# Kernel optimization log

Measured on AMD Instinct MI355X. Metric: run time of the kernel, lower is better.

The kernel has to match this reference:

```python
import jax, jax.numpy as jnp
import numpy as np

B, C, H, W, K = 4, 32, 192, 192, 3
BETA = 15.0   # soft-max temperature used by the repo's Morphology module
EPS = 1e-5    # BatchNorm eps
KK = K * K


def _window_taps(x, dil):
    """Zero-padded dilated KxK window taps, stacked on axis 0 -> (KK, B, C, H, W).
    Matches nn.Unfold(kernel_size=K, dilation=dil, padding=dil*(K//2))."""
    p = dil * (K // 2)
    xp = jnp.pad(x, ((0, 0), (0, 0), (p, p), (p, p)))
    return jnp.stack(
        [xp[:, :, i * dil:i * dil + H, j * dil:j * dil + W]
         for i in range(K) for j in range(K)], axis=0)


def _w_taps(w):
    # (C, K, K) -> (KK, 1, C, 1, 1) aligned with tap order i*K+j
    return w.reshape(C, KK).T[:, None, :, None, None]


def soft_dilate(x, w, dil):
    v = _window_taps(x, dil) + _w_taps(w)          # (KK,B,C,H,W)
    return jax.nn.logsumexp(BETA * v, axis=0) / BETA


def soft_erode(x, w, dil):
    v = _w_taps(w) - _window_taps(x, dil)
    return -(jax.nn.logsumexp(BETA * v, axis=0) / BETA)


def batchnorm(x, gamma, beta):
    mu = jnp.mean(x, axis=(0, 2, 3), keepdims=True)
    var = jnp.var(x, axis=(0, 2, 3), keepdims=True)
    xn = (x - mu) * jax.lax.rsqrt(var + EPS)
    return xn * gamma[None, :, None, None] + beta[None, :, None, None]


def setup_inputs() -> dict:
    key = jax.random.key(0)
    k1, k2, k3, k4 = jax.random.split(key, 4)
    return {
        "x": jax.random.normal(k1, (B, C, H, W), jnp.float32),
        "wd": jax.random.normal(k2, (4, C, K, K), jnp.float32) * 0.1,
        "we": jax.random.normal(k3, (4, C, K, K), jnp.float32) * 0.1,
        "gs": jnp.ones((4, C), jnp.float32),
        "bs": jnp.zeros((4, C), jnp.float32),
        "Wc": jax.random.normal(k4, (C, 4 * C), jnp.float32) * (1.0 / np.sqrt(4 * C)),
        "g": jnp.ones((C,), jnp.float32),
        "b": jnp.zeros((C,), jnp.float32),
    }


def reference(x, wd, we, gs, bs, Wc, g, b):
    branches = []
    for i in range(4):                      # fixed set of dilation factors 1..4
        d = i + 1
        y = soft_dilate(x, wd[i], d)        # soft morphological dilation
        y = soft_erode(y, we[i], d)         # then erosion => closing
        y = jax.nn.relu(batchnorm(y, gs[i], bs[i]))
        branches.append(y)
    xc = jnp.concatenate(branches, axis=1)  # (B, 4C, H, W)
    y = jnp.einsum('bihw,oi->bohw', xc, Wc) # 1x1 conv, no bias
    y = jax.nn.relu(batchnorm(y, g, b))
    return y                                 # Dropout2d is identity in eval
```

## Files before the change

kernel.cpp:

```cpp
#include <hip/hip_runtime.h>
#include <hip/hip_bf16.h>

#define B_   4
#define C_   32
#define H_   192
#define W_   192
#define HW_  (H_ * W_)
#define EPS_ 1e-5f

#define SCALE_IN  21.640425613334453f
#define SCALE_OUT 0.046209812037329687f

#define SPW 48
#define SQW 40

#define NP1 (128 * 288)
#define NP2 (32 * 288)

__device__ __forceinline__ float bf2f(unsigned short u) {
    return __uint_as_float((unsigned int)u << 16);
}
__device__ __forceinline__ unsigned short f2bf(float f) {
    const unsigned int u = __float_as_uint(f);
    return (unsigned short)((u + 0x7fffu + ((u >> 16) & 1u)) >> 16);
}

__device__ float          g_cw[2304];
__device__ float          g_Wt[4096];
__device__ float          g_stats[320];
__device__ float          g_p1[2 * NP1];
__device__ float          g_p2[2 * NP2];
__device__ __attribute__((aligned(16))) unsigned short g_E[(size_t)4 * B_ * C_ * HW_];
__device__ __attribute__((aligned(16))) unsigned short g_Yb[(size_t)B_ * C_ * HW_];

__global__ void prep_k(const float* __restrict__ wd, const float* __restrict__ we,
                       const float* __restrict__ Wc) {
    for (int i = threadIdx.x; i < 2304; i += 256) {
        const float v = (i < 1152) ? wd[i] : we[i - 1152];
        g_cw[i] = exp2f(SCALE_IN * v);
    }
    for (int i = threadIdx.x; i < 4096; i += 256) {
        const int ci = i >> 5;
        const int k  = i & 31;
        g_Wt[i] = Wc[(size_t)k * 128 + ci];
    }
}

template<int D>
__device__ __forceinline__ void morph_branch(int b, int c, int h0, int w0,
                                             int slotbase,
                                             const float* __restrict__ sP,
                                             float* __restrict__ sQ) {
    constexpr int QE    = 32 + 2 * D;
    constexpr int QEG8  = (QE + 7) / 8;
    constexpr int UNITS = QE * QEG8;
    constexpr int POFF  = 8 - 2 * D;
    constexpr int AB    = POFF & ~3;
    constexpr int OFF   = POFF & 3;
    constexpr int NR    = (OFF + 2 * D + 8 + 3) / 4;
    constexpr int NR3   = (2 * D + 8 + 3) / 4;
    constexpr int br    = D - 1;

    const int tid = threadIdx.x;
    const int cb  = (br * C_ + c) * 9;

    if (tid < UNITS) {
        float cd[9];
#pragma unroll
        for (int k = 0; k < 9; k++) cd[k] = g_cw[cb + k];

        const int qi = tid / QEG8;
        const int qj = (tid - qi * QEG8) * 8;
        float a[8];
#pragma unroll
        for (int u = 0; u < 8; u++) a[u] = 0.f;

#pragma unroll
        for (int i = 0; i < 3; i++) {
            const float* rp = &sP[(qi + 8 + (i - 2) * D) * SPW + qj + AB];
            float buf[NR * 4];
#pragma unroll
            for (int r = 0; r < NR; r++)
                *(float4*)&buf[r * 4] = *(const float4*)&rp[r * 4];
#pragma unroll
            for (int j = 0; j < 3; j++) {
                const float wgt = cd[i * 3 + j];
#pragma unroll
                for (int u = 0; u < 8; u++)
                    a[u] = fmaf(wgt, buf[OFF + j * D + u], a[u]);
            }
        }
        const int hq = h0 - D + qi;
        const bool rowo = (hq < 0) || (hq >= H_);
        float q[8];
#pragma unroll
        for (int u = 0; u < 8; u++) {
            float qq = __builtin_amdgcn_rcpf(a[u]);
            const int wq = w0 - D + qj + u;
            q[u] = (rowo || (wq < 0) || (wq >= W_)) ? 1.0f : qq;
        }
        *(float4*)&sQ[qi * SQW + qj]     = make_float4(q[0], q[1], q[2], q[3]);
        *(float4*)&sQ[qi * SQW + qj + 4] = make_float4(q[4], q[5], q[6], q[7]);
    }
    __syncthreads();

    if (tid < 128) {
        float ce[9];
#pragma unroll
        for (int k = 0; k < 9; k++) ce[k] = g_cw[1152 + cb + k];

        const int oi = tid >> 2;
        const int oj = (tid & 3) * 8;
        float t[8];
#pragma unroll
        for (int u = 0; u < 8; u++) t[u] = 0.f;

#pragma unroll
        for (int i = 0; i < 3; i++) {
            const float* rq = &sQ[(oi + i * D) * SQW + oj];
            float buf[NR3 * 4];
#pragma unroll
            for (int r = 0; r < NR3; r++)
                *(float4*)&buf[r * 4] = *(const float4*)&rq[r * 4];
#pragma unroll
            for (int j = 0; j < 3; j++) {
                const float wgt = ce[i * 3 + j];
#pragma unroll
                for (int u = 0; u < 8; u++)
                    t[u] = fmaf(wgt, buf[j * D + u], t[u]);
            }
        }
        float e[8];
#pragma unroll
        for (int u = 0; u < 8; u++) e[u] = -SCALE_OUT * log2f(t[u]);

        uint4 pk;
        pk.x = (unsigned int)f2bf(e[0]) | ((unsigned int)f2bf(e[1]) << 16);
        pk.y = (unsigned int)f2bf(e[2]) | ((unsigned int)f2bf(e[3]) << 16);
        pk.z = (unsigned int)f2bf(e[4]) | ((unsigned int)f2bf(e[5]) << 16);
        pk.w = (unsigned int)f2bf(e[6]) | ((unsigned int)f2bf(e[7]) << 16);
        *(uint4*)&g_E[(((size_t)br * B_ + b) * C_ + c) * HW_
                      + (size_t)(h0 + oi) * W_ + w0 + oj] = pk;

        float s1 = 0.f, s2 = 0.f;
#pragma unroll
        for (int u = 0; u < 8; u++) { s1 += e[u]; s2 += e[u] * e[u]; }
#pragma unroll
        for (int off = 32; off >= 1; off >>= 1) {
            s1 += __shfl_down(s1, off, 64);
            s2 += __shfl_down(s2, off, 64);
        }
        if ((tid & 63) == 0) {
            const int slot = (br * C_ + c) * 288 + slotbase + (tid >> 6);
            g_p1[slot]       = s1;
            g_p1[NP1 + slot] = s2;
        }
    }
    __syncthreads();
}

__global__ __launch_bounds__(256) void morph_k(const float* __restrict__ x) {
    __shared__ float sP[48 * SPW];
    __shared__ float sQ[40 * SQW];
    const int tile = blockIdx.x;
    const int c    = blockIdx.y;
    const int b    = blockIdx.z;
    const int th   = tile / 6;
    const int tw   = tile - th * 6;
    const int h0   = th * 32, w0 = tw * 32;

    const float* xm = x + (size_t)(b * C_ + c) * HW_;
    for (int idx = threadIdx.x; idx < 48 * 48; idx += 256) {
        const int r  = idx / 48, q = idx - r * 48;
        const int ih = h0 - 8 + r, iw = w0 - 8 + q;
        const int ihc = min(max(ih, 0), H_ - 1);
        const int iwc = min(max(iw, 0), W_ - 1);
        const float xv = xm[ihc * W_ + iwc];
        const bool inb = (ih == ihc) && (iw == iwc);
        sP[r * SPW + q] = inb ? exp2f(SCALE_IN * xv) : 1.0f;
    }
    __syncthreads();

    const int slotbase = (b * 36 + tile) * 2;
    morph_branch<1>(b, c, h0, w0, slotbase, sP, sQ);
    morph_branch<2>(b, c, h0, w0, slotbase, sP, sQ);
    morph_branch<3>(b, c, h0, w0, slotbase, sP, sQ);
    morph_branch<4>(b, c, h0, w0, slotbase, sP, sQ);
}

__global__ __launch_bounds__(256) void fin1_k(const float* __restrict__ gs,
                                              const float* __restrict__ bs) {
    const int chan = blockIdx.x;
    const int base = chan * 288;
    float s1 = 0.0f, s2 = 0.0f;
    for (int i = threadIdx.x; i < 288; i += 256) {
        s1 += g_p1[base + i];
        s2 += g_p1[NP1 + base + i];
    }
#pragma unroll
    for (int off = 32; off >= 1; off >>= 1) {
        s1 += __shfl_down(s1, off, 64);
        s2 += __shfl_down(s2, off, 64);
    }
    __shared__ float l1[4], l2[4];
    const int lane = threadIdx.x & 63;
    const int wv   = threadIdx.x >> 6;
    if (lane == 0) { l1[wv] = s1; l2[wv] = s2; }
    __syncthreads();
    if (threadIdx.x == 0) {
        const float S1 = l1[0] + l1[1] + l1[2] + l1[3];
        const float S2 = l2[0] + l2[1] + l2[2] + l2[3];
        const float N  = (float)(B_ * HW_);
        const float mu = S1 / N;
        const float va = fmaxf(S2 / N - mu * mu, 0.0f);
        const float sc = gs[chan] * rsqrtf(va + EPS_);
        g_stats[chan]       = sc;
        g_stats[128 + chan] = bs[chan] - mu * sc;
    }
}

__global__ __launch_bounds__(256) void conv_k(void) {
    const int og = blockIdx.y;
    const int b  = blockIdx.z;
    const int p  = (blockIdx.x * 256 + threadIdx.x) * 2;

    float acc0[8], acc1[8];
#pragma unroll
    for (int k = 0; k < 8; k++) { acc0[k] = 0.0f; acc1[k] = 0.0f; }

#pragma unroll 8
    for (int ci = 0; ci < 128; ci++) {
        const int br = ci >> 5;
        const int c  = ci & 31;
        const unsigned int eu =
            *(const unsigned int*)&g_E[(((size_t)br * B_ + b) * C_ + c) * HW_ + p];
        float v0 = __uint_as_float(eu << 16);
        float v1 = __uint_as_float(eu & 0xffff0000u);
        const float sc = g_stats[ci], sh = g_stats[128 + ci];
        v0 = fmaxf(fmaf(v0, sc, sh), 0.0f);
        v1 = fmaxf(fmaf(v1, sc, sh), 0.0f);
        const float* wr = &g_Wt[ci * 32 + og * 8];
#pragma unroll
        for (int k = 0; k < 8; k++) {
            acc0[k] = fmaf(v0, wr[k], acc0[k]);
            acc1[k] = fmaf(v1, wr[k], acc1[k]);
        }
    }

    unsigned short* Yp = g_Yb + ((size_t)b * C_ + og * 8) * HW_ + p;
#pragma unroll
    for (int k = 0; k < 8; k++) {
        const unsigned int pack =
            (unsigned int)f2bf(acc0[k]) | ((unsigned int)f2bf(acc1[k]) << 16);
        *(unsigned int*)&Yp[(size_t)k * HW_] = pack;
    }

    __shared__ float l1[8][4], l2[8][4];
    const int lane = threadIdx.x & 63;
    const int wv   = threadIdx.x >> 6;
#pragma unroll
    for (int k = 0; k < 8; k++) {
        float s1 = acc0[k] + acc1[k];
        float s2 = acc0[k] * acc0[k] + acc1[k] * acc1[k];
#pragma unroll
        for (int off = 32; off >= 1; off >>= 1) {
            s1 += __shfl_down(s1, off, 64);
            s2 += __shfl_down(s2, off, 64);
        }
        if (lane == 0) { l1[k][wv] = s1; l2[k][wv] = s2; }
    }
    __syncthreads();
    if (threadIdx.x < 8) {
        const int k = threadIdx.x;
        const int chan = og * 8 + k;
        const int slot = chan * 288 + b * 72 + blockIdx.x;
        g_p2[slot]       = l1[k][0] + l1[k][1] + l1[k][2] + l1[k][3];
        g_p2[NP2 + slot] = l2[k][0] + l2[k][1] + l2[k][2] + l2[k][3];
    }
}

__global__ __launch_bounds__(256) void fin2_k(const float* __restrict__ g,
                                              const float* __restrict__ bb) {
    const int chan = blockIdx.x;
    const int base = chan * 288;
    float s1 = 0.0f, s2 = 0.0f;
    for (int i = threadIdx.x; i < 288; i += 256) {
        s1 += g_p2[base + i];
        s2 += g_p2[NP2 + base + i];
    }
#pragma unroll
    for (int off = 32; off >= 1; off >>= 1) {
        s1 += __shfl_down(s1, off, 64);
        s2 += __shfl_down(s2, off, 64);
    }
    __shared__ float l1[4], l2[4];
    const int lane = threadIdx.x & 63;
    const int wv   = threadIdx.x >> 6;
    if (lane == 0) { l1[wv] = s1; l2[wv] = s2; }
    __syncthreads();
    if (threadIdx.x == 0) {
        const float S1 = l1[0] + l1[1] + l1[2] + l1[3];
        const float S2 = l2[0] + l2[1] + l2[2] + l2[3];
        const float N  = (float)(B_ * HW_);
        const float mu = S1 / N;
        const float va = fmaxf(S2 / N - mu * mu, 0.0f);
        const float sc = g[chan] * rsqrtf(va + EPS_);
        g_stats[256 + chan] = sc;
        g_stats[288 + chan] = bb[chan] - mu * sc;
    }
}

__global__ __launch_bounds__(256) void final_k(float* __restrict__ out) {
    const int c = blockIdx.y;
    const int b = blockIdx.z;
    const size_t base = (size_t)(b * C_ + c) * HW_ + (blockIdx.x * 256 + threadIdx.x) * 8;
    const float sc = g_stats[256 + c];
    const float sh = g_stats[288 + c];
    const uint4 u = *(const uint4*)&g_Yb[base];

    float4 r0, r1;
    r0.x = fmaxf(fmaf(__uint_as_float(u.x << 16),         sc, sh), 0.0f);
    r0.y = fmaxf(fmaf(__uint_as_float(u.x & 0xffff0000u), sc, sh), 0.0f);
    r0.z = fmaxf(fmaf(__uint_as_float(u.y << 16),         sc, sh), 0.0f);
    r0.w = fmaxf(fmaf(__uint_as_float(u.y & 0xffff0000u), sc, sh), 0.0f);
    r1.x = fmaxf(fmaf(__uint_as_float(u.z << 16),         sc, sh), 0.0f);
    r1.y = fmaxf(fmaf(__uint_as_float(u.z & 0xffff0000u), sc, sh), 0.0f);
    r1.z = fmaxf(fmaf(__uint_as_float(u.w << 16),         sc, sh), 0.0f);
    r1.w = fmaxf(fmaf(__uint_as_float(u.w & 0xffff0000u), sc, sh), 0.0f);

    *(float4*)&out[base]     = r0;
    *(float4*)&out[base + 4] = r1;
}

extern "C" void kernel_launch(void* const* d_in, const int* in_sizes, int n_in,
                              void* d_out, int out_size, void* d_ws, size_t ws_size,
                              hipStream_t stream) {
    const float* x  = (const float*)d_in[0];
    const float* wd = (const float*)d_in[1];
    const float* we = (const float*)d_in[2];
    const float* gs = (const float*)d_in[3];
    const float* bs = (const float*)d_in[4];
    const float* Wc = (const float*)d_in[5];
    const float* g  = (const float*)d_in[6];
    const float* bb = (const float*)d_in[7];

    prep_k<<<1, 256, 0, stream>>>(wd, we, Wc);
    morph_k<<<dim3(36, C_, B_), 256, 0, stream>>>(x);
    fin1_k<<<128, 256, 0, stream>>>(gs, bs);
    conv_k<<<dim3(HW_ / 512, 4, B_), 256, 0, stream>>>();
    fin2_k<<<32, 256, 0, stream>>>(g, bb);
    final_k<<<dim3(HW_ / 2048, C_, B_), 256, 0, stream>>>((float*)d_out);
}
```

Baseline: 106.1 us.

## Process two channels per morph block with packed FMA; widen conv output group

The morphology kernel now handles two channels per block. Their exp-domain tiles are interleaved in shared memory so each thread can use two-wide vector FMAs (packed fp32) over 4 pixels, and all 256 threads take part in the erosion stage. Partial-stat slots double to match. The 1x1 conv kernel now computes 16 output channels per thread instead of 8, halving the number of E re-reads but doubling accumulator registers and cutting the grid in half.

```diff
diff --git a/kernel.cpp b/kernel.cpp
--- a/kernel.cpp
+++ b/kernel.cpp
@@ -11,11 +11,13 @@
 #define SCALE_IN  21.640425613334453f
 #define SCALE_OUT 0.046209812037329687f
 
-#define SPW 48
-#define SQW 40
-
-#define NP1 (128 * 288)
+#define SPF 96
+#define SQF 80
+
+#define NP1 (128 * 576)
 #define NP2 (32 * 288)
+
+typedef float vf2 __attribute__((ext_vector_type(2)));
 
 __device__ __forceinline__ float bf2f(unsigned short u) {
     return __uint_as_float((unsigned int)u << 16);
@@ -47,153 +49,179 @@
 }
 
 template<int D>
-__device__ __forceinline__ void morph_branch(int b, int c, int h0, int w0,
+__device__ __forceinline__ void morph_branch(int b, int c0, int h0, int w0,
                                              int slotbase,
-                                             const float* __restrict__ sP,
-                                             float* __restrict__ sQ) {
+                                             const float* __restrict__ sPf,
+                                             float* __restrict__ sQf) {
     constexpr int QE    = 32 + 2 * D;
-    constexpr int QEG8  = (QE + 7) / 8;
-    constexpr int UNITS = QE * QEG8;
+    constexpr int QEG   = (QE + 3) / 4;
+    constexpr int UNITS = QE * QEG;
     constexpr int POFF  = 8 - 2 * D;
-    constexpr int AB    = POFF & ~3;
-    constexpr int OFF   = POFF & 3;
-    constexpr int NR    = (OFF + 2 * D + 8 + 3) / 4;
-    constexpr int NR3   = (2 * D + 8 + 3) / 4;
+    constexpr int NRF   = D + 2;
     constexpr int br    = D - 1;
 
     const int tid = threadIdx.x;
-    const int cb  = (br * C_ + c) * 9;
-
-    if (tid < UNITS) {
-        float cd[9];
-#pragma unroll
-        for (int k = 0; k < 9; k++) cd[k] = g_cw[cb + k];
-
-        const int qi = tid / QEG8;
-        const int qj = (tid - qi * QEG8) * 8;
-        float a[8];
-#pragma unroll
-        for (int u = 0; u < 8; u++) a[u] = 0.f;
+    const int cb0 = (br * C_ + c0) * 9;
+
+    vf2 cdv[9], cev[9];
+#pragma unroll
+    for (int k = 0; k < 9; k++) {
+        cdv[k] = (vf2){g_cw[cb0 + k],        g_cw[cb0 + 9 + k]};
+        cev[k] = (vf2){g_cw[1152 + cb0 + k], g_cw[1152 + cb0 + 9 + k]};
+    }
+
+#pragma unroll
+    for (int it = 0; it < 2; ++it) {
+        const int unit = tid + it * 256;
+        if (unit < UNITS) {
+            const int qi = unit / QEG;
+            const int qj = (unit - qi * QEG) * 4;
+            vf2 a[4];
+#pragma unroll
+            for (int u = 0; u < 4; u++) a[u] = (vf2){0.f, 0.f};
+
+#pragma unroll
+            for (int i = 0; i < 3; i++) {
+                const float* rp = &sPf[(qi + 8 + (i - 2) * D) * SPF
+                                       + 2 * (qj + POFF)];
+                float buf[NRF * 4];
+#pragma unroll
+                for (int r = 0; r < NRF; r++)
+                    *(float4*)&buf[r * 4] = *(const float4*)&rp[r * 4];
+#pragma unroll
+                for (int j = 0; j < 3; j++) {
+                    const vf2 w = cdv[i * 3 + j];
+#pragma unroll
+                    for (int u = 0; u < 4; u++) {
+                        const vf2 p = (vf2){buf[2 * (j * D + u)],
+                                            buf[2 * (j * D + u) + 1]};
+                        a[u] = __builtin_elementwise_fma(w, p, a[u]);
+                    }
+                }
+            }
+            const int hq = h0 - D + qi;
+            const bool rowo = (hq < 0) || (hq >= H_);
+            vf2 q[4];
+#pragma unroll
+            for (int u = 0; u < 4; u++) {
+                vf2 qq;
+                qq.x = __builtin_amdgcn_rcpf(a[u].x);
+                qq.y = __builtin_amdgcn_rcpf(a[u].y);
+                const int wq = w0 - D + qj + u;
+                if (rowo || (wq < 0) || (wq >= W_)) qq = (vf2){1.f, 1.f};
+                q[u] = qq;
+            }
+            float* dst = &sQf[qi * SQF + 2 * qj];
+            *(float4*)&dst[0] = make_float4(q[0].x, q[0].y, q[1].x, q[1].y);
+            *(float4*)&dst[4] = make_float4(q[2].x, q[2].y, q[3].x, q[3].y);
+        }
+    }
+    __syncthreads();
+
+    {
+        const int oi = tid >> 3;
+        const int oj = (tid & 7) * 4;
+        vf2 t[4];
+#pragma unroll
+        for (int u = 0; u < 4; u++) t[u] = (vf2){0.f, 0.f};
 
 #pragma unroll
         for (int i = 0; i < 3; i++) {
-            const float* rp = &sP[(qi + 8 + (i - 2) * D) * SPW + qj + AB];
-            float buf[NR * 4];
-#pragma unroll
-            for (int r = 0; r < NR; r++)
-                *(float4*)&buf[r * 4] = *(const float4*)&rp[r * 4];
+            const float* rq = &sQf[(oi + i * D) * SQF + 2 * oj];
+            float buf[NRF * 4];
+#pragma unroll
+            for (int r = 0; r < NRF; r++)
+                *(float4*)&buf[r * 4] = *(const float4*)&rq[r * 4];
 #pragma unroll
             for (int j = 0; j < 3; j++) {
-                const float wgt = cd[i * 3 + j];
-#pragma unroll
-                for (int u = 0; u < 8; u++)
-                    a[u] = fmaf(wgt, buf[OFF + j * D + u], a[u]);
+                const vf2 w = cev[i * 3 + j];
+#pragma unroll
+                for (int u = 0; u < 4; u++) {
+                    const vf2 p = (vf2){buf[2 * (j * D + u)],
+                                        buf[2 * (j * D + u) + 1]};
+                    t[u] = __builtin_elementwise_fma(w, p, t[u]);
+                }
             }
         }
-        const int hq = h0 - D + qi;
-        const bool rowo = (hq < 0) || (hq >= H_);
-        float q[8];
-#pragma unroll
-        for (int u = 0; u < 8; u++) {
-            float qq = __builtin_amdgcn_rcpf(a[u]);
-            const int wq = w0 - D + qj + u;
-            q[u] = (rowo || (wq < 0) || (wq >= W_)) ? 1.0f : qq;
-        }
-        *(float4*)&sQ[qi * SQW + qj]     = make_float4(q[0], q[1], q[2], q[3]);
-        *(float4*)&sQ[qi * SQW + qj + 4] = make_float4(q[4], q[5], q[6], q[7]);
-    }
-    __syncthreads();
-
-    if (tid < 128) {
-        float ce[9];
-#pragma unroll
-        for (int k = 0; k < 9; k++) ce[k] = g_cw[1152 + cb + k];
-
-        const int oi = tid >> 2;
-        const int oj = (tid & 3) * 8;
-        float t[8];
-#pragma unroll
-        for (int u = 0; u < 8; u++) t[u] = 0.f;
-
-#pragma unroll
-        for (int i = 0; i < 3; i++) {
-            const float* rq = &sQ[(oi + i * D) * SQW + oj];
-            float buf[NR3 * 4];
-#pragma unroll
-            for (int r = 0; r < NR3; r++)
-                *(float4*)&buf[r * 4] = *(const float4*)&rq[r * 4];
-#pragma unroll
-            for (int j = 0; j < 3; j++) {
-                const float wgt = ce[i * 3 + j];
-#pragma unroll
-                for (int u = 0; u < 8; u++)
-                    t[u] = fmaf(wgt, buf[j * D + u], t[u]);
-            }
-        }
-        float e[8];
-#pragma unroll
-        for (int u = 0; u < 8; u++) e[u] = -SCALE_OUT * log2f(t[u]);
-
-        uint4 pk;
-        pk.x = (unsigned int)f2bf(e[0]) | ((unsigned int)f2bf(e[1]) << 16);
-        pk.y = (unsigned int)f2bf(e[2]) | ((unsigned int)f2bf(e[3]) << 16);
-        pk.z = (unsigned int)f2bf(e[4]) | ((unsigned int)f2bf(e[5]) << 16);
-        pk.w = (unsigned int)f2bf(e[6]) | ((unsigned int)f2bf(e[7]) << 16);
-        *(uint4*)&g_E[(((size_t)br * B_ + b) * C_ + c) * HW_
-                      + (size_t)(h0 + oi) * W_ + w0 + oj] = pk;
-
-        float s1 = 0.f, s2 = 0.f;
-#pragma unroll
-        for (int u = 0; u < 8; u++) { s1 += e[u]; s2 += e[u] * e[u]; }
+        vf2 e[4];
+#pragma unroll
+        for (int u = 0; u < 4; u++) {
+            e[u].x = -SCALE_OUT * log2f(t[u].x);
+            e[u].y = -SCALE_OUT * log2f(t[u].y);
+        }
+
+        const size_t eb = (((size_t)br * B_ + b) * C_ + c0) * HW_
+                          + (size_t)(h0 + oi) * W_ + w0 + oj;
+        ushort4 r0, r1;
+        r0.x = f2bf(e[0].x); r0.y = f2bf(e[1].x);
+        r0.z = f2bf(e[2].x); r0.w = f2bf(e[3].x);
+        r1.x = f2bf(e[0].y); r1.y = f2bf(e[1].y);
+        r1.z = f2bf(e[2].y); r1.w = f2bf(e[3].y);
+        *(ushort4*)&g_E[eb]       = r0;
+        *(ushort4*)&g_E[eb + HW_] = r1;
+
+        float s1x = e[0].x + e[1].x + e[2].x + e[3].x;
+        float s2x = e[0].x * e[0].x + e[1].x * e[1].x
+                  + e[2].x * e[2].x + e[3].x * e[3].x;
+        float s1y = e[0].y + e[1].y + e[2].y + e[3].y;
+        float s2y = e[0].y * e[0].y + e[1].y * e[1].y
+                  + e[2].y * e[2].y + e[3].y * e[3].y;
 #pragma unroll
         for (int off = 32; off >= 1; off >>= 1) {
-            s1 += __shfl_down(s1, off, 64);
-            s2 += __shfl_down(s2, off, 64);
+            s1x += __shfl_down(s1x, off, 64);
+            s2x += __shfl_down(s2x, off, 64);
+            s1y += __shfl_down(s1y, off, 64);
+            s2y += __shfl_down(s2y, off, 64);
         }
         if ((tid & 63) == 0) {
-            const int slot = (br * C_ + c) * 288 + slotbase + (tid >> 6);
-            g_p1[slot]       = s1;
-            g_p1[NP1 + slot] = s2;
+            const int wv = tid >> 6;
+            const int slot0 = (br * C_ + c0) * 576 + slotbase + wv;
+            g_p1[slot0]             = s1x;
+            g_p1[NP1 + slot0]       = s2x;
+            g_p1[slot0 + 576]       = s1y;
+            g_p1[NP1 + slot0 + 576] = s2y;
         }
     }
     __syncthreads();
 }
 
 __global__ __launch_bounds__(256) void morph_k(const float* __restrict__ x) {
-    __shared__ float sP[48 * SPW];
-    __shared__ float sQ[40 * SQW];
+    __shared__ float sPf[48 * SPF];
+    __shared__ float sQf[40 * SQF];
     const int tile = blockIdx.x;
-    const int c    = blockIdx.y;
+    const int c0   = blockIdx.y * 2;
     const int b    = blockIdx.z;
     const int th   = tile / 6;
     const int tw   = tile - th * 6;
     const int h0   = th * 32, w0 = tw * 32;
 
-    const float* xm = x + (size_t)(b * C_ + c) * HW_;
+    const float* xm0 = x + (size_t)(b * C_ + c0) * HW_;
+    const float* xm1 = xm0 + HW_;
     for (int idx = threadIdx.x; idx < 48 * 48; idx += 256) {
         const int r  = idx / 48, q = idx - r * 48;
         const int ih = h0 - 8 + r, iw = w0 - 8 + q;
         const int ihc = min(max(ih, 0), H_ - 1);
         const int iwc = min(max(iw, 0), W_ - 1);
-        const float xv = xm[ihc * W_ + iwc];
         const bool inb = (ih == ihc) && (iw == iwc);
-        sP[r * SPW + q] = inb ? exp2f(SCALE_IN * xv) : 1.0f;
-    }
-    __syncthreads();
-
-    const int slotbase = (b * 36 + tile) * 2;
-    morph_branch<1>(b, c, h0, w0, slotbase, sP, sQ);
-    morph_branch<2>(b, c, h0, w0, slotbase, sP, sQ);
-    morph_branch<3>(b, c, h0, w0, slotbase, sP, sQ);
-    morph_branch<4>(b, c, h0, w0, slotbase, sP, sQ);
+        const float v0 = inb ? exp2f(SCALE_IN * xm0[ihc * W_ + iwc]) : 1.0f;
+        const float v1 = inb ? exp2f(SCALE_IN * xm1[ihc * W_ + iwc]) : 1.0f;
+        *(float2*)&sPf[r * SPF + 2 * q] = make_float2(v0, v1);
+    }
+    __syncthreads();
+
+    const int slotbase = (b * 36 + tile) * 4;
+    morph_branch<1>(b, c0, h0, w0, slotbase, sPf, sQf);
+    morph_branch<2>(b, c0, h0, w0, slotbase, sPf, sQf);
+    morph_branch<3>(b, c0, h0, w0, slotbase, sPf, sQf);
+    morph_branch<4>(b, c0, h0, w0, slotbase, sPf, sQf);
 }
 
 __global__ __launch_bounds__(256) void fin1_k(const float* __restrict__ gs,
                                               const float* __restrict__ bs) {
     const int chan = blockIdx.x;
-    const int base = chan * 288;
+    const int base = chan * 576;
     float s1 = 0.0f, s2 = 0.0f;
-    for (int i = threadIdx.x; i < 288; i += 256) {
+    for (int i = threadIdx.x; i < 576; i += 256) {
         s1 += g_p1[base + i];
         s2 += g_p1[NP1 + base + i];
     }
@@ -224,11 +252,11 @@
     const int b  = blockIdx.z;
     const int p  = (blockIdx.x * 256 + threadIdx.x) * 2;
 
-    float acc0[8], acc1[8];
-#pragma unroll
-    for (int k = 0; k < 8; k++) { acc0[k] = 0.0f; acc1[k] = 0.0f; }
-
-#pragma unroll 8
+    float acc0[16], acc1[16];
+#pragma unroll
+    for (int k = 0; k < 16; k++) { acc0[k] = 0.0f; acc1[k] = 0.0f; }
+
+#pragma unroll 4
     for (int ci = 0; ci < 128; ci++) {
         const int br = ci >> 5;
         const int c  = ci & 31;
@@ -239,27 +267,27 @@
         const float sc = g_stats[ci], sh = g_stats[128 + ci];
         v0 = fmaxf(fmaf(v0, sc, sh), 0.0f);
         v1 = fmaxf(fmaf(v1, sc, sh), 0.0f);
-        const float* wr = &g_Wt[ci * 32 + og * 8];
-#pragma unroll
-        for (int k = 0; k < 8; k++) {
+        const float* wr = &g_Wt[ci * 32 + og * 16];
+#pragma unroll
+        for (int k = 0; k < 16; k++) {
             acc0[k] = fmaf(v0, wr[k], acc0[k]);
             acc1[k] = fmaf(v1, wr[k], acc1[k]);
         }
     }
 
-    unsigned short* Yp = g_Yb + ((size_t)b * C_ + og * 8) * HW_ + p;
-#pragma unroll
-    for (int k = 0; k < 8; k++) {
+    unsigned short* Yp = g_Yb + ((size_t)b * C_ + og * 16) * HW_ + p;
+#pragma unroll
+    for (int k = 0; k < 16; k++) {
         const unsigned int pack =
             (unsigned int)f2bf(acc0[k]) | ((unsigned int)f2bf(acc1[k]) << 16);
         *(unsigned int*)&Yp[(size_t)k * HW_] = pack;
     }
 
-    __shared__ float l1[8][4], l2[8][4];
+    __shared__ float l1[16][4], l2[16][4];
     const int lane = threadIdx.x & 63;
     const int wv   = threadIdx.x >> 6;
 #pragma unroll
-    for (int k = 0; k < 8; k++) {
+    for (int k = 0; k < 16; k++) {
         float s1 = acc0[k] + acc1[k];
         float s2 = acc0[k] * acc0[k] + acc1[k] * acc1[k];
 #pragma unroll
@@ -270,9 +298,9 @@
         if (lane == 0) { l1[k][wv] = s1; l2[k][wv] = s2; }
     }
     __syncthreads();
-    if (threadIdx.x < 8) {
+    if (threadIdx.x < 16) {
         const int k = threadIdx.x;
-        const int chan = og * 8 + k;
+        const int chan = og * 16 + k;
         const int slot = chan * 288 + b * 72 + blockIdx.x;
         g_p2[slot]       = l1[k][0] + l1[k][1] + l1[k][2] + l1[k][3];
         g_p2[NP2 + slot] = l2[k][0] + l2[k][1] + l2[k][2] + l2[k][3];
@@ -345,9 +373,9 @@
     const float* bb = (const float*)d_in[7];
 
     prep_k<<<1, 256, 0, stream>>>(wd, we, Wc);
-    morph_k<<<dim3(36, C_, B_), 256, 0, stream>>>(x);
+    morph_k<<<dim3(36, 16, B_), 256, 0, stream>>>(x);
     fin1_k<<<128, 256, 0, stream>>>(gs, bs);
-    conv_k<<<dim3(HW_ / 512, 4, B_), 256, 0, stream>>>();
+    conv_k<<<dim3(HW_ / 512, 2, B_), 256, 0, stream>>>();
     fin2_k<<<32, 256, 0, stream>>>(g, bb);
     final_k<<<dim3(HW_ / 2048, C_, B_), 256, 0, stream>>>((float*)d_out);
 }
```

Result: slower. 114.1 us (+7.5%).
